# Kernel optimization log

Measured on AMD Instinct MI355X. Metric: run time of the kernel, lower is better.

Reference implementation:

```python
import jax, jax.numpy as jnp
import numpy as np

HID = 768
PATCH = 32
IMG = 384
PD = IMG // PATCH          # 12
NPATCH = PD * PD           # 144
MAXLEN = 144               # config.max_image_length (== num_patches)
VOCAB = 30522
SEQ = 40
B = 64
EPS = 1e-12


def _layernorm(x, g, b):
    mu = jnp.mean(x, axis=-1, keepdims=True)
    var = jnp.mean(jnp.square(x - mu), axis=-1, keepdims=True)
    return (x - mu) / jnp.sqrt(var + EPS) * g + b


def _bilinear_pad(sp, h, w, out_h, out_w):
    # sp: [C, PD, PD]; bilinear (align_corners=True) resize to (h, w), zero-pad to (out_h, out_w)
    pd = sp.shape[1]
    hf = jnp.maximum(h - 1, 1).astype(jnp.float32)
    wf = jnp.maximum(w - 1, 1).astype(jnp.float32)
    ry = jnp.arange(out_h, dtype=jnp.float32) * (pd - 1) / hf
    rx = jnp.arange(out_w, dtype=jnp.float32) * (pd - 1) / wf
    y0 = jnp.clip(jnp.floor(ry).astype(jnp.int32), 0, pd - 1)
    x0 = jnp.clip(jnp.floor(rx).astype(jnp.int32), 0, pd - 1)
    y1 = jnp.minimum(y0 + 1, pd - 1)
    x1 = jnp.minimum(x0 + 1, pd - 1)
    wy = (ry - y0.astype(jnp.float32))[:, None]   # [out_h,1]
    wx = (rx - x0.astype(jnp.float32))[None, :]   # [1,out_w]
    a = sp[:, y0][:, :, x0]
    b = sp[:, y0][:, :, x1]
    c = sp[:, y1][:, :, x0]
    d = sp[:, y1][:, :, x1]
    val = a * (1 - wy) * (1 - wx) + b * (1 - wy) * wx + c * wy * (1 - wx) + d * wy * wx
    valid = (jnp.arange(out_h)[:, None] < h) & (jnp.arange(out_w)[None, :] < w)
    return val * valid  # [C,out_h,out_w]


def setup_inputs():
    key = jax.random.key(0)
    ks = jax.random.split(key, 12)
    s = 0.02
    return {
        "input_ids": jax.random.randint(ks[0], (B, SEQ), 0, VOCAB, dtype=jnp.int32),
        "attention_mask": jnp.ones((B, SEQ), dtype=jnp.int32),
        "token_type_ids": jnp.zeros((B, SEQ), dtype=jnp.int32),
        "pixel_values": jax.random.normal(ks[1], (B, 3, IMG, IMG), jnp.float32),
        "pixel_mask": jnp.ones((B, IMG, IMG), dtype=jnp.int32),
        "word_emb": jax.random.normal(ks[2], (VOCAB, HID), jnp.float32) * s,
        "pos_emb_text": jax.random.normal(ks[3], (SEQ, HID), jnp.float32) * s,
        "tok_type_emb": jax.random.normal(ks[4], (2, HID), jnp.float32) * s,
        "ln_gamma": jnp.ones((HID,), jnp.float32),
        "ln_beta": jnp.zeros((HID,), jnp.float32),
        "cls_token": jax.random.normal(ks[5], (1, 1, HID), jnp.float32) * s,
        "conv_w": jax.random.normal(ks[6], (HID, 3, PATCH, PATCH), jnp.float32) * s,
        "conv_b": jnp.zeros((HID,), jnp.float32),
        "vis_pos_emb": jax.random.normal(ks[7], (1, NPATCH + 1, HID), jnp.float32) * s,
        "modality_emb": jax.random.normal(ks[8], (2, HID), jnp.float32) * s,
        "image_token_type_idx": 1,
    }


def reference(input_ids, attention_mask, token_type_ids, pixel_values, pixel_mask,
              word_emb, pos_emb_text, tok_type_emb, ln_gamma, ln_beta, cls_token,
              conv_w, conv_b, vis_pos_emb, modality_emb, image_token_type_idx):
    bsz, seq = input_ids.shape

    # ---- text embeddings ----
    te = word_emb[input_ids] + tok_type_emb[token_type_ids] + pos_emb_text[None, :seq]
    te = _layernorm(te, ln_gamma, ln_beta)

    # ---- patch conv projection ----
    x = jax.lax.conv_general_dilated(
        pixel_values, conv_w, (PATCH, PATCH), 'VALID',
        dimension_numbers=('NCHW', 'OIHW', 'NCHW')) + conv_b[None, :, None, None]
    _, C, H, W = x.shape

    # ---- nearest-downsample pixel mask to patch grid ----
    iy = (jnp.arange(H) * (pixel_mask.shape[1] // H))
    ix = (jnp.arange(W) * (pixel_mask.shape[2] // W))
    xm = pixel_mask[:, iy][:, :, ix]          # [B,H,W] int
    x_h = xm.sum(axis=1)[:, 0]                # valid rows per image
    x_w = xm.sum(axis=2)[:, 0]                # valid cols per image

    # ---- per-sample bilinear interp of spatial position embeddings ----
    sp = vis_pos_emb[0, 1:].T.reshape(C, PD, PD)
    pos = jax.vmap(lambda h, w: _bilinear_pad(sp, h, w, H, W))(x_h, x_w)  # [B,C,H,W]

    # ---- deterministic gather: valid patches first (original order), then invalid pads ----
    N = H * W
    mask_flat = xm.reshape(bsz, N)
    keys = (1 - mask_flat) * (N + 1) + jnp.arange(N)[None, :]
    sel = jnp.argsort(keys, axis=1)[:, :MAXLEN]                 # [B,L]

    x_tok = jnp.take_along_axis(x.reshape(bsz, C, N).transpose(0, 2, 1), sel[:, :, None], axis=1)
    pos_tok = jnp.take_along_axis(pos.reshape(bsz, C, N).transpose(0, 2, 1), sel[:, :, None], axis=1)
    m_tok = jnp.take_along_axis(mask_flat, sel, axis=1)

    cls = jnp.broadcast_to(cls_token, (bsz, 1, C))
    pos_cls = jnp.broadcast_to(vis_pos_emb[:, :1], (bsz, 1, C))
    x_img = jnp.concatenate([cls, x_tok], axis=1) + jnp.concatenate([pos_cls, pos_tok], axis=1)
    m_img = jnp.concatenate([jnp.ones((bsz, 1), m_tok.dtype), m_tok], axis=1)

    # ---- modality (token-type) embeddings ----
    te = te + modality_emb[0][None, None, :]
    x_img = x_img + modality_emb[image_token_type_idx][None, None, :]

    embeddings = jnp.concatenate([te, x_img], axis=1)           # [B, seq+1+L, HID]
    masks = jnp.concatenate([attention_mask.astype(jnp.int32), m_img.astype(jnp.int32)], axis=1)
    return embeddings, masks
```

## Files before the change

### kernel.cpp

```cpp
#include <hip/hip_runtime.h>
#include <hip/hip_bf16.h>
#include <stdint.h>

typedef __hip_bfloat16 bf16;
typedef __bf16 bf16x8 __attribute__((ext_vector_type(8)));
typedef float f32x4 __attribute__((ext_vector_type(4)));
typedef unsigned short u16x8 __attribute__((ext_vector_type(8)));

#define HID   768
#define SEQL  40
#define TOK   185
#define NP    144
#define PD2   12
#define KDIM  3072
#define IMGSZ 384
#define IMG2  147456

#define WSB_PIX 0
#define WSB_W   56623104
#define WSB_INT 61341696
#define WS_DST 0
#define WS_SRC 9216
#define WS_MV  18432
#define WS_XH  27648
#define WS_XW  27712

#define EMB_ELEMS (64 * TOK * HID)

__device__ __forceinline__ unsigned short f2bu(float x) {
    uint32_t u = __float_as_uint(x);
    return (unsigned short)((u + 0x7FFFu + ((u >> 16) & 1u)) >> 16);
}

__global__ __launch_bounds__(256) void cast_f32_bf16(const float* __restrict__ in,
                                                     unsigned short* __restrict__ out, int n8) {
    for (int i = blockIdx.x * 256 + threadIdx.x; i < n8; i += gridDim.x * 256) {
        f32x4 a = ((const f32x4*)in)[2 * i];
        f32x4 b = ((const f32x4*)in)[2 * i + 1];
        u16x8 r;
#pragma unroll
        for (int j = 0; j < 4; j++) r[j] = f2bu(a[j]);
#pragma unroll
        for (int j = 0; j < 4; j++) r[4 + j] = f2bu(b[j]);
        ((u16x8*)out)[i] = r;
    }
}

__global__ __launch_bounds__(256) void aux_kernel(
    const int* __restrict__ ids, const int* __restrict__ tts,
    const float* __restrict__ wemb, const float* __restrict__ ptext,
    const float* __restrict__ ttemb, const float* __restrict__ g,
    const float* __restrict__ be, const float* __restrict__ modal,
    const int* __restrict__ pmask, const float* __restrict__ cls,
    const float* __restrict__ vpos, const int* __restrict__ tti,
    const int* __restrict__ attn, int* __restrict__ ws,
    float* __restrict__ out) {
    int bid = blockIdx.x, tid = threadIdx.x;
    if (bid < 64 * SEQL) {
        int b = bid / SEQL, s = bid % SEQL;
        int id = ids[b * SEQL + s];
        int tt = tts[b * SEQL + s];
        const float* wr = wemb + (size_t)id * HID;
        const float* tr = ttemb + (size_t)tt * HID;
        const float* pr = ptext + s * HID;
        float x[3], s1 = 0.f, s2 = 0.f;
#pragma unroll
        for (int k = 0; k < 3; k++) {
            int n = tid + k * 256;
            float xv = wr[n] + tr[n] + pr[n];
            x[k] = xv; s1 += xv; s2 += xv * xv;
        }
        for (int off = 32; off; off >>= 1) {
            s1 += __shfl_down(s1, off);
            s2 += __shfl_down(s2, off);
        }
        __shared__ float red[8];
        int lane = tid & 63, wid = tid >> 6;
        if (lane == 0) { red[wid] = s1; red[4 + wid] = s2; }
        __syncthreads();
        float ts1 = red[0] + red[1] + red[2] + red[3];
        float ts2 = red[4] + red[5] + red[6] + red[7];
        float mu = ts1 * (1.0f / HID);
        float var = ts2 * (1.0f / HID) - mu * mu;
        float rstd = rsqrtf(var + 1e-12f);
        float* orow = out + ((size_t)(b * TOK + s)) * HID;
#pragma unroll
        for (int k = 0; k < 3; k++) {
            int n = tid + k * 256;
            orow[n] = (x[k] - mu) * rstd * g[n] + be[n] + modal[n];
        }
    } else if (bid < 64 * SEQL + 64) {
        int b = bid - 64 * SEQL;
        __shared__ int v[NP];
        if (tid < NP) {
            int i = tid / PD2, j = tid % PD2;
            v[tid] = pmask[(size_t)b * IMG2 + (size_t)(i * 32) * IMGSZ + (j * 32)];
        }
        __syncthreads();
        if (tid == 0) {
            int nv = 0;
            for (int p = 0; p < NP; p++) nv += (v[p] != 0);
            int cv = 0, ci = 0;
            for (int p = 0; p < NP; p++) {
                int d = v[p] ? (cv++) : (nv + ci++);
                ws[WS_DST + b * NP + p] = d;
                ws[WS_SRC + b * NP + d] = p;
                ws[WS_MV + b * NP + p] = v[p];
            }
            int h = 0, w = 0;
            for (int i = 0; i < PD2; i++) h += v[i * PD2];
            for (int j = 0; j < PD2; j++) w += v[j];
            ws[WS_XH + b] = h;
            ws[WS_XW + b] = w;
        }
    } else {
        int b = bid - (64 * SEQL + 64);
        int tt = *tti;
        const float* modalr = modal + tt * HID;
        float* orow = out + ((size_t)(b * TOK + SEQL)) * HID;
#pragma unroll
        for (int k = 0; k < 3; k++) {
            int n = tid + k * 256;
            orow[n] = cls[n] + vpos[n] + modalr[n];
        }
        __shared__ int v2[NP];
        if (tid < NP) {
            int i = tid / PD2, j = tid % PD2;
            v2[tid] = pmask[(size_t)b * IMG2 + (size_t)(i * 32) * IMGSZ + (j * 32)];
        }
        __syncthreads();
        __shared__ int srcl[NP];
        if (tid == 0) {
            int nv = 0;
            for (int p = 0; p < NP; p++) nv += (v2[p] != 0);
            int cv = 0, ci = 0;
            for (int p = 0; p < NP; p++) {
                int d = v2[p] ? (cv++) : (nv + ci++);
                srcl[d] = p;
            }
        }
        __syncthreads();
        float* om = out + (size_t)EMB_ELEMS + (size_t)b * TOK;
        if (tid < TOK) {
            float mv;
            if (tid < SEQL) mv = (float)attn[b * SEQL + tid];
            else if (tid == SEQL) mv = 1.0f;
            else mv = (float)v2[srcl[tid - (SEQL + 1)]];
            om[tid] = mv;
        }
    }
}

__global__ __launch_bounds__(256, 2) void gemm_kernel(
    const bf16* __restrict__ pix, const bf16* __restrict__ W,
    const float* __restrict__ bias, const float* __restrict__ vpos,
    const float* __restrict__ modal, const int* __restrict__ tti,
    const int* __restrict__ ws, float* __restrict__ out) {
    __shared__ unsigned short As[2 * 128 * 64];
    __shared__ unsigned short Bs[2 * 128 * 64];

    int bid = blockIdx.x;
    int swz = (bid & 7) * 54 + (bid >> 3);
    int bm = swz / 6, bn = swz - bm * 6;
    int m0 = bm << 7, n0 = bn << 7;

    int tid = threadIdx.x;
    int lane = tid & 63, wid = tid >> 6;
    int wm = wid >> 1, wn = wid & 1;

    int kof = (tid & 7) << 3;
    size_t apix[4]; size_t wbase[4]; int kofs[4];
#pragma unroll
    for (int r = 0; r < 4; r++) {
        int row = (tid >> 3) + r * 32;
        kofs[r] = kof ^ ((row & 7) << 3);
        int gm = m0 + row;
        int b_ = gm / NP; int p_ = gm - b_ * NP;
        int ii = p_ / PD2, jj = p_ - ii * PD2;
        apix[r] = (size_t)(b_ * 3) * IMG2 + (size_t)(ii * 32) * IMGSZ + (jj * 32);
        wbase[r] = (size_t)(n0 + row) * KDIM + kofs[r];
    }

    f32x4 acc[4][4];
#pragma unroll
    for (int a = 0; a < 4; a++)
#pragma unroll
        for (int c = 0; c < 4; c++) acc[a][c] = (f32x4){0.f, 0.f, 0.f, 0.f};

#define STAGE(BUF, KT)                                                              \
    {                                                                               \
        _Pragma("unroll")                                                           \
        for (int r = 0; r < 4; r++) {                                               \
            int k = (KT) + kofs[r];                                                 \
            int ci = k >> 10; int rem = k & 1023;                                   \
            size_t cioff = (size_t)ci * IMG2 + (size_t)(rem >> 5) * IMGSZ + (rem & 31); \
            const bf16* ga = pix + apix[r] + cioff;                                 \
            const bf16* gb = W + wbase[r] + (KT);                                   \
            unsigned short* la = As + (BUF) * 8192 + r * 2048 + wid * 512;          \
            unsigned short* lb = Bs + (BUF) * 8192 + r * 2048 + wid * 512;          \
            __builtin_amdgcn_global_load_lds(                                       \
                (const __attribute__((address_space(1))) unsigned int*)ga,          \
                (__attribute__((address_space(3))) unsigned int*)la, 16, 0, 0);     \
            __builtin_amdgcn_global_load_lds(                                       \
                (const __attribute__((address_space(1))) unsigned int*)gb,          \
                (__attribute__((address_space(3))) unsigned int*)lb, 16, 0, 0);     \
        }                                                                           \
    }

    STAGE(0, 0);
    for (int kt = 0; kt < KDIM; kt += 64) {
        int buf = (kt >> 6) & 1;
        __syncthreads();
        if (kt + 64 < KDIM) STAGE(buf ^ 1, kt + 64);
#pragma unroll
        for (int ks = 0; ks < 2; ks++) {
            int kb = (ks << 5) + ((lane >> 4) << 3);
            bf16x8 af[4], bfr[4];
#pragma unroll
            for (int mi = 0; mi < 4; mi++) {
                int row = (wm << 6) + (mi << 4) + (lane & 15);
                af[mi] = *(const bf16x8*)&As[buf * 8192 + row * 64 + (kb ^ ((row & 7) << 3))];
            }
#pragma unroll
            for (int nj = 0; nj < 4; nj++) {
                int row = (wn << 6) + (nj << 4) + (lane & 15);
                bfr[nj] = *(const bf16x8*)&Bs[buf * 8192 + row * 64 + (kb ^ ((row & 7) << 3))];
            }
#pragma unroll
            for (int mi = 0; mi < 4; mi++)
#pragma unroll
                for (int nj = 0; nj < 4; nj++)
                    acc[mi][nj] = __builtin_amdgcn_mfma_f32_16x16x32_bf16(
                        af[mi], bfr[nj], acc[mi][nj], 0, 0, 0);
        }
    }
#undef STAGE

    int tt = *tti;
    const float* modalr = modal + tt * HID;
    int r16 = lane >> 4, c16 = lane & 15;
#pragma unroll
    for (int mi = 0; mi < 4; mi++) {
#pragma unroll
        for (int reg = 0; reg < 4; reg++) {
            int gm = m0 + (wm << 6) + (mi << 4) + (r16 << 2) + reg;
            int b_ = gm / NP; int p_ = gm - b_ * NP;
            int ii = p_ / PD2, jj = p_ - ii * PD2;
            int h = ws[WS_XH + b_], w = ws[WS_XW + b_];
            float hf = (float)((h - 1) > 1 ? (h - 1) : 1);
            float wf = (float)((w - 1) > 1 ? (w - 1) : 1);
            float ry = (float)(ii * (PD2 - 1)) / hf;
            float rx = (float)(jj * (PD2 - 1)) / wf;
            int y0 = (int)floorf(ry); y0 = y0 < 0 ? 0 : (y0 > PD2 - 1 ? PD2 - 1 : y0);
            int x0 = (int)floorf(rx); x0 = x0 < 0 ? 0 : (x0 > PD2 - 1 ? PD2 - 1 : x0);
            int y1 = y0 + 1 > PD2 - 1 ? PD2 - 1 : y0 + 1;
            int x1 = x0 + 1 > PD2 - 1 ? PD2 - 1 : x0 + 1;
            float wy = ry - (float)y0, wx = rx - (float)x0;
            float vs = ((ii < h) && (jj < w)) ? 1.0f : 0.0f;
            float w00 = (1.f - wy) * (1.f - wx) * vs, w01 = (1.f - wy) * wx * vs;
            float w10 = wy * (1.f - wx) * vs, w11 = wy * wx * vs;
            const float* p00 = vpos + (size_t)(1 + y0 * PD2 + x0) * HID;
            const float* p01 = vpos + (size_t)(1 + y0 * PD2 + x1) * HID;
            const float* p10 = vpos + (size_t)(1 + y1 * PD2 + x0) * HID;
            const float* p11 = vpos + (size_t)(1 + y1 * PD2 + x1) * HID;
            int drow = ws[WS_DST + b_ * NP + p_];
            float* orow = out + ((size_t)(b_ * TOK + SEQL + 1 + drow)) * HID;
#pragma unroll
            for (int nj = 0; nj < 4; nj++) {
                int n = n0 + (wn << 6) + (nj << 4) + c16;
                float pos = w00 * p00[n] + w01 * p01[n] + w10 * p10[n] + w11 * p11[n];
                orow[n] = acc[mi][nj][reg] + bias[n] + pos + modalr[n];
            }
        }
    }
}

extern "C" void kernel_launch(void* const* d_in, const int* in_sizes, int n_in,
                              void* d_out, int out_size, void* d_ws, size_t ws_size,
                              hipStream_t stream) {
    const int* ids = (const int*)d_in[0];
    const int* attn = (const int*)d_in[1];
    const int* tts = (const int*)d_in[2];
    const float* pix = (const float*)d_in[3];
    const int* pmask = (const int*)d_in[4];
    const float* wemb = (const float*)d_in[5];
    const float* ptext = (const float*)d_in[6];
    const float* ttemb = (const float*)d_in[7];
    const float* g = (const float*)d_in[8];
    const float* be = (const float*)d_in[9];
    const float* cls = (const float*)d_in[10];
    const float* Wc = (const float*)d_in[11];
    const float* bias = (const float*)d_in[12];
    const float* vpos = (const float*)d_in[13];
    const float* modal = (const float*)d_in[14];
    const int* tti = (const int*)d_in[15];
    float* out = (float*)d_out;

    unsigned short* pixb = (unsigned short*)((char*)d_ws + WSB_PIX);
    unsigned short* wb = (unsigned short*)((char*)d_ws + WSB_W);
    int* wsi = (int*)((char*)d_ws + WSB_INT);

    cast_f32_bf16<<<2048, 256, 0, stream>>>(pix, pixb, 28311552 / 8);
    cast_f32_bf16<<<512, 256, 0, stream>>>(Wc, wb, 2359296 / 8);
    aux_kernel<<<64 * SEQL + 128, 256, 0, stream>>>(ids, tts, wemb, ptext, ttemb, g, be,
                                                    modal, pmask, cls, vpos, tti, attn, wsi, out);
    gemm_kernel<<<432, 256, 0, stream>>>((const bf16*)pixb, (const bf16*)wb,
                                         bias, vpos, modal, tti, wsi, out);
}
```

Measured before the change: 109.6 us.

## Fuse pixel fp32-to-bf16 cast into GEMM A-tile loading

Drops the separate cast kernel that converted all pixel values to bf16 in workspace. The GEMM now loads fp32 pixels into registers for the next K-tile, overlaps that with MFMA compute on the current tile, then converts to bf16 and writes into swizzled LDS. This removes a full write and re-read of the bf16 pixel copy. The cost is more registers and VGPR-staged loads instead of direct global-to-LDS loads for A.

```diff
diff --git a/kernel.cpp b/kernel.cpp
--- a/kernel.cpp
+++ b/kernel.cpp
@@ -16,9 +16,8 @@
 #define IMGSZ 384
 #define IMG2  147456
 
-#define WSB_PIX 0
-#define WSB_W   56623104
-#define WSB_INT 61341696
+#define WSB_W   0
+#define WSB_INT 4718592
 #define WS_DST 0
 #define WS_SRC 9216
 #define WS_MV  18432
@@ -152,7 +151,7 @@
 }
 
 __global__ __launch_bounds__(256, 2) void gemm_kernel(
-    const bf16* __restrict__ pix, const bf16* __restrict__ W,
+    const float* __restrict__ pixf, const bf16* __restrict__ W,
     const float* __restrict__ bias, const float* __restrict__ vpos,
     const float* __restrict__ modal, const int* __restrict__ tti,
     const int* __restrict__ ws, float* __restrict__ out) {
@@ -169,10 +168,11 @@
     int wm = wid >> 1, wn = wid & 1;
 
     int kof = (tid & 7) << 3;
-    size_t apix[4]; size_t wbase[4]; int kofs[4];
+    size_t apix[4]; size_t wbase[4]; int kofs[4]; int rowr[4];
 #pragma unroll
     for (int r = 0; r < 4; r++) {
         int row = (tid >> 3) + r * 32;
+        rowr[r] = row;
         kofs[r] = kof ^ ((row & 7) << 3);
         int gm = m0 + row;
         int b_ = gm / NP; int p_ = gm - b_ * NP;
@@ -187,54 +187,91 @@
 #pragma unroll
         for (int c = 0; c < 4; c++) acc[a][c] = (f32x4){0.f, 0.f, 0.f, 0.f};
 
-#define STAGE(BUF, KT)                                                              \
+    f32x4 areg[4][2];
+
+#define LOADA(KT)                                                                   \
     {                                                                               \
         _Pragma("unroll")                                                           \
         for (int r = 0; r < 4; r++) {                                               \
-            int k = (KT) + kofs[r];                                                 \
+            int k = (KT) + kof;              \
             int ci = k >> 10; int rem = k & 1023;                                   \
             size_t cioff = (size_t)ci * IMG2 + (size_t)(rem >> 5) * IMGSZ + (rem & 31); \
-            const bf16* ga = pix + apix[r] + cioff;                                 \
+            const float* ga = pixf + apix[r] + cioff;                               \
+            areg[r][0] = *(const f32x4*)ga;                                         \
+            areg[r][1] = *(const f32x4*)(ga + 4);                                   \
+        }                                                                           \
+    }
+
+#define WRITEA(BUF)                                                                 \
+    {                                                                               \
+        _Pragma("unroll")                                                           \
+        for (int r = 0; r < 4; r++) {                                               \
+            u16x8 pk;                                                               \
+            _Pragma("unroll")                                                       \
+            for (int j = 0; j < 4; j++) pk[j] = f2bu(areg[r][0][j]);                \
+            _Pragma("unroll")                                                       \
+            for (int j = 0; j < 4; j++) pk[4 + j] = f2bu(areg[r][1][j]);            \
+            *(u16x8*)&As[(BUF) * 8192 + rowr[r] * 64 + kofs[r]] = pk;               \
+        }                                                                           \
+    }
+
+#define STAGEB(BUF, KT)                                                             \
+    {                                                                               \
+        _Pragma("unroll")                                                           \
+        for (int r = 0; r < 4; r++) {                                               \
             const bf16* gb = W + wbase[r] + (KT);                                   \
-            unsigned short* la = As + (BUF) * 8192 + r * 2048 + wid * 512;          \
             unsigned short* lb = Bs + (BUF) * 8192 + r * 2048 + wid * 512;          \
-            __builtin_amdgcn_global_load_lds(                                       \
-                (const __attribute__((address_space(1))) unsigned int*)ga,          \
-                (__attribute__((address_space(3))) unsigned int*)la, 16, 0, 0);     \
             __builtin_amdgcn_global_load_lds(                                       \
                 (const __attribute__((address_space(1))) unsigned int*)gb,          \
                 (__attribute__((address_space(3))) unsigned int*)lb, 16, 0, 0);     \
         }                                                                           \
     }
 
-    STAGE(0, 0);
+#define COMPUTE(BUF)                                                                \
+    {                                                                               \
+        _Pragma("unroll")                                                           \
+        for (int ks = 0; ks < 2; ks++) {                                            \
+            int kb = (ks << 5) + ((lane >> 4) << 3);                                \
+            bf16x8 af[4], bfr[4];                                                   \
+            _Pragma("unroll")                                                       \
+            for (int mi = 0; mi < 4; mi++) {                                        \
+                int row = (wm << 6) + (mi << 4) + (lane & 15);                      \
+                af[mi] = *(const bf16x8*)&As[(BUF) * 8192 + row * 64 + (kb ^ ((row & 7) << 3))]; \
+            }                                                                       \
+            _Pragma("unroll")                                                       \
+            for (int nj = 0; nj < 4; nj++) {                                        \
+                int row = (wn << 6) + (nj << 4) + (lane & 15);                      \
+                bfr[nj] = *(const bf16x8*)&Bs[(BUF) * 8192 + row * 64 + (kb ^ ((row & 7) << 3))]; \
+            }                                                                       \
+            _Pragma("unroll")                                                       \
+            for (int mi = 0; mi < 4; mi++)                                          \
+                _Pragma("unroll")                                                   \
+                for (int nj = 0; nj < 4; nj++)                                      \
+                    acc[mi][nj] = __builtin_amdgcn_mfma_f32_16x16x32_bf16(          \
+                        af[mi], bfr[nj], acc[mi][nj], 0, 0, 0);                     \
+        }                                                                           \
+    }
+
+    LOADA(0);
+    STAGEB(0, 0);
+    WRITEA(0);
+    __syncthreads();
     for (int kt = 0; kt < KDIM; kt += 64) {
         int buf = (kt >> 6) & 1;
-        __syncthreads();
-        if (kt + 64 < KDIM) STAGE(buf ^ 1, kt + 64);
-#pragma unroll
-        for (int ks = 0; ks < 2; ks++) {
-            int kb = (ks << 5) + ((lane >> 4) << 3);
-            bf16x8 af[4], bfr[4];
-#pragma unroll
-            for (int mi = 0; mi < 4; mi++) {
-                int row = (wm << 6) + (mi << 4) + (lane & 15);
-                af[mi] = *(const bf16x8*)&As[buf * 8192 + row * 64 + (kb ^ ((row & 7) << 3))];
-            }
-#pragma unroll
-            for (int nj = 0; nj < 4; nj++) {
-                int row = (wn << 6) + (nj << 4) + (lane & 15);
-                bfr[nj] = *(const bf16x8*)&Bs[buf * 8192 + row * 64 + (kb ^ ((row & 7) << 3))];
-            }
-#pragma unroll
-            for (int mi = 0; mi < 4; mi++)
-#pragma unroll
-                for (int nj = 0; nj < 4; nj++)
-                    acc[mi][nj] = __builtin_amdgcn_mfma_f32_16x16x32_bf16(
-                        af[mi], bfr[nj], acc[mi][nj], 0, 0, 0);
-        }
-    }
-#undef STAGE
+        if (kt + 64 < KDIM) {
+            LOADA(kt + 64);
+            STAGEB(buf ^ 1, kt + 64);
+            COMPUTE(buf);
+            WRITEA(buf ^ 1);
+        } else {
+            COMPUTE(buf);
+        }
+        __syncthreads();
+    }
+#undef LOADA
+#undef WRITEA
+#undef STAGEB
+#undef COMPUTE
 
     int tt = *tti;
     const float* modalr = modal + tt * HID;
@@ -296,14 +333,12 @@
     const int* tti = (const int*)d_in[15];
     float* out = (float*)d_out;
 
-    unsigned short* pixb = (unsigned short*)((char*)d_ws + WSB_PIX);
     unsigned short* wb = (unsigned short*)((char*)d_ws + WSB_W);
     int* wsi = (int*)((char*)d_ws + WSB_INT);
 
-    cast_f32_bf16<<<2048, 256, 0, stream>>>(pix, pixb, 28311552 / 8);
-    cast_f32_bf16<<<512, 256, 0, stream>>>(Wc, wb, 2359296 / 8);
+    cast_f32_bf16<<<1152, 256, 0, stream>>>(Wc, wb, 2359296 / 8);
     aux_kernel<<<64 * SEQL + 128, 256, 0, stream>>>(ids, tts, wemb, ptext, ttemb, g, be,
                                                     modal, pmask, cls, vpos, tti, attn, wsi, out);
-    gemm_kernel<<<432, 256, 0, stream>>>((const bf16*)pixb, (const bf16*)wb,
+    gemm_kernel<<<432, 256, 0, stream>>>(pix, (const bf16*)wb,
                                          bias, vpos, modal, tti, wsi, out);
 }
```

Measured after the change: 111.5 us. Within noise of the previous version (+1.7%).

## Load GEMM weight operand directly into registers, bypassing LDS staging

Applied to the files above, without the earlier changes.

The weight (B) tile is no longer staged through shared memory. Each wave now loads its MFMA B fragments straight from global memory into double-buffered registers, while the pixel (A) tile still goes through LDS via global_load_lds. The main loop is unrolled by two so the register buffers alternate. This removes the B LDS writes and reads and halves the shared-memory footprint. In exchange it duplicates weight loads across waves that share columns, uses strided per-row accesses that coalesce poorly, and adds about 64 VGPRs of register pressure.

```diff
diff --git a/kernel.cpp b/kernel.cpp
--- a/kernel.cpp
+++ b/kernel.cpp
@@ -157,7 +157,6 @@
     const float* __restrict__ modal, const int* __restrict__ tti,
     const int* __restrict__ ws, float* __restrict__ out) {
     __shared__ unsigned short As[2 * 128 * 64];
-    __shared__ unsigned short Bs[2 * 128 * 64];
 
     int bid = blockIdx.x;
     int swz = (bid & 7) * 54 + (bid >> 3);
@@ -169,7 +168,7 @@
     int wm = wid >> 1, wn = wid & 1;
 
     int kof = (tid & 7) << 3;
-    size_t apix[4]; size_t wbase[4]; int kofs[4];
+    size_t apix[4]; int kofs[4];
 #pragma unroll
     for (int r = 0; r < 4; r++) {
         int row = (tid >> 3) + r * 32;
@@ -178,7 +177,13 @@
         int b_ = gm / NP; int p_ = gm - b_ * NP;
         int ii = p_ / PD2, jj = p_ - ii * PD2;
         apix[r] = (size_t)(b_ * 3) * IMG2 + (size_t)(ii * 32) * IMGSZ + (jj * 32);
-        wbase[r] = (size_t)(n0 + row) * KDIM + kofs[r];
+    }
+
+    const bf16* baddr[4];
+#pragma unroll
+    for (int nj = 0; nj < 4; nj++) {
+        int row = n0 + (wn << 6) + (nj << 4) + (lane & 15);
+        baddr[nj] = W + (size_t)row * KDIM + ((lane >> 4) << 3);
     }
 
     f32x4 acc[4][4];
@@ -187,7 +192,9 @@
 #pragma unroll
         for (int c = 0; c < 4; c++) acc[a][c] = (f32x4){0.f, 0.f, 0.f, 0.f};
 
-#define STAGE(BUF, KT)                                                              \
+    bf16x8 BA[8], BB[8];
+
+#define STAGEA(BUF, KT)                                                             \
     {                                                                               \
         _Pragma("unroll")                                                           \
         for (int r = 0; r < 4; r++) {                                               \
@@ -195,46 +202,56 @@
             int ci = k >> 10; int rem = k & 1023;                                   \
             size_t cioff = (size_t)ci * IMG2 + (size_t)(rem >> 5) * IMGSZ + (rem & 31); \
             const bf16* ga = pix + apix[r] + cioff;                                 \
-            const bf16* gb = W + wbase[r] + (KT);                                   \
             unsigned short* la = As + (BUF) * 8192 + r * 2048 + wid * 512;          \
-            unsigned short* lb = Bs + (BUF) * 8192 + r * 2048 + wid * 512;          \
             __builtin_amdgcn_global_load_lds(                                       \
                 (const __attribute__((address_space(1))) unsigned int*)ga,          \
                 (__attribute__((address_space(3))) unsigned int*)la, 16, 0, 0);     \
-            __builtin_amdgcn_global_load_lds(                                       \
-                (const __attribute__((address_space(1))) unsigned int*)gb,          \
-                (__attribute__((address_space(3))) unsigned int*)lb, 16, 0, 0);     \
         }                                                                           \
     }
 
-    STAGE(0, 0);
-    for (int kt = 0; kt < KDIM; kt += 64) {
-        int buf = (kt >> 6) & 1;
-        __syncthreads();
-        if (kt + 64 < KDIM) STAGE(buf ^ 1, kt + 64);
-#pragma unroll
-        for (int ks = 0; ks < 2; ks++) {
-            int kb = (ks << 5) + ((lane >> 4) << 3);
-            bf16x8 af[4], bfr[4];
-#pragma unroll
-            for (int mi = 0; mi < 4; mi++) {
-                int row = (wm << 6) + (mi << 4) + (lane & 15);
-                af[mi] = *(const bf16x8*)&As[buf * 8192 + row * 64 + (kb ^ ((row & 7) << 3))];
-            }
-#pragma unroll
-            for (int nj = 0; nj < 4; nj++) {
-                int row = (wn << 6) + (nj << 4) + (lane & 15);
-                bfr[nj] = *(const bf16x8*)&Bs[buf * 8192 + row * 64 + (kb ^ ((row & 7) << 3))];
-            }
-#pragma unroll
-            for (int mi = 0; mi < 4; mi++)
-#pragma unroll
-                for (int nj = 0; nj < 4; nj++)
-                    acc[mi][nj] = __builtin_amdgcn_mfma_f32_16x16x32_bf16(
-                        af[mi], bfr[nj], acc[mi][nj], 0, 0, 0);
-        }
-    }
-#undef STAGE
+#define LOADB(REG, KT)                                                              \
+    {                                                                               \
+        _Pragma("unroll")                                                           \
+        for (int nj = 0; nj < 4; nj++) {                                            \
+            REG[nj * 2 + 0] = *(const bf16x8*)(baddr[nj] + (KT));                   \
+            REG[nj * 2 + 1] = *(const bf16x8*)(baddr[nj] + (KT) + 32);              \
+        }                                                                           \
+    }
+
+#define COMPUTE(BUF, REG)                                                           \
+    {                                                                               \
+        _Pragma("unroll")                                                           \
+        for (int ks = 0; ks < 2; ks++) {                                            \
+            int kb = (ks << 5) + ((lane >> 4) << 3);                                \
+            bf16x8 af[4];                                                           \
+            _Pragma("unroll")                                                       \
+            for (int mi = 0; mi < 4; mi++) {                                        \
+                int row = (wm << 6) + (mi << 4) + (lane & 15);                      \
+                af[mi] = *(const bf16x8*)&As[(BUF) * 8192 + row * 64 + (kb ^ ((row & 7) << 3))]; \
+            }                                                                       \
+            _Pragma("unroll")                                                       \
+            for (int mi = 0; mi < 4; mi++)                                          \
+                _Pragma("unroll")                                                   \
+                for (int nj = 0; nj < 4; nj++)                                      \
+                    acc[mi][nj] = __builtin_amdgcn_mfma_f32_16x16x32_bf16(          \
+                        af[mi], REG[nj * 2 + ks], acc[mi][nj], 0, 0, 0);            \
+        }                                                                           \
+    }
+
+    STAGEA(0, 0);
+    LOADB(BA, 0);
+    __syncthreads();
+    for (int kt2 = 0; kt2 < KDIM; kt2 += 128) {
+        if (kt2 + 64 < KDIM) { STAGEA(1, kt2 + 64); LOADB(BB, kt2 + 64); }
+        COMPUTE(0, BA);
+        __syncthreads();
+        if (kt2 + 128 < KDIM) { STAGEA(0, kt2 + 128); LOADB(BA, kt2 + 128); }
+        if (kt2 + 64 < KDIM) COMPUTE(1, BB);
+        __syncthreads();
+    }
+#undef STAGEA
+#undef LOADB
+#undef COMPUTE
 
     int tt = *tti;
     const float* modalr = modal + tt * HID;
```

Measured after the change: 179.9 us. +64.1%, slower.
